# Kernel optimization log

Measured on AMD Instinct MI355X. Metric: run time of the kernel, lower is better.

The kernel has to match this reference:

```python
import jax, jax.numpy as jnp
import numpy as np

NKV = 8      # n_head_kv
G = 8        # n_head // n_head_kv
D = 64       # head_dim (hardcoded in source views)
NH = NKV * G # n_head = 64


def rotate_half(x):
    x1, x2 = x[..., : D // 2], x[..., D // 2:]
    return jnp.concatenate((-x2, x1), axis=-1)


def setup_inputs() -> dict:
    key = jax.random.key(0)
    ks = jax.random.split(key, 9)
    B, S, H = 2, 1024, 4096
    hidden_states = jax.random.normal(ks[0], (B, S, H), dtype=jnp.float32)
    alibi = jnp.zeros((B * NH, 1, S), dtype=jnp.float32)            # unused in this forward path
    attention_mask = jnp.zeros((B, 1, S, S), dtype=jnp.float32)      # unused (is_causal=True)
    cos = jax.random.uniform(ks[1], (S, D), dtype=jnp.float32, minval=-1.0, maxval=1.0)
    sin = jax.random.uniform(ks[2], (S, D), dtype=jnp.float32, minval=-1.0, maxval=1.0)
    wq = jax.random.normal(ks[3], (H, H), dtype=jnp.float32) * 0.02          # Linear weight (out, in)
    wk = jax.random.normal(ks[4], (NKV * D, H), dtype=jnp.float32) * 0.02
    wv = jax.random.normal(ks[5], (NKV * D, H), dtype=jnp.float32) * 0.02
    wd = jax.random.normal(ks[6], (H, H), dtype=jnp.float32) * 0.02          # dense weight
    return {"hidden_states": hidden_states, "alibi": alibi, "attention_mask": attention_mask,
            "cos": cos, "sin": sin, "wq": wq, "wk": wk, "wv": wv, "wd": wd}


def reference(hidden_states, alibi, attention_mask, cos, sin, wq, wk, wv, wd):
    B, S, H = hidden_states.shape
    # fused-style projections (Linear: x @ W.T, no bias)
    # q: [B, S, NKV, G, D] -> [B, NKV, G, S, D]; head h = kv_group*G + j (group-major, matches source rearrange)
    q = (hidden_states @ wq.T).reshape(B, S, NKV, G, D).transpose(0, 2, 3, 1, 4)
    k = (hidden_states @ wk.T).reshape(B, S, NKV, D).transpose(0, 2, 1, 3)   # [B, NKV, S, D]
    v = (hidden_states @ wv.T).reshape(B, S, NKV, D).transpose(0, 2, 1, 3)
    # RoPE (cos/sin broadcast over batch/head dims)
    q = q * cos + rotate_half(q) * sin
    k = k * cos + rotate_half(k) * sin
    # grouped-query attention without materializing broadcast K/V
    inv_norm = jnp.asarray(1.0 / np.sqrt(D), dtype=hidden_states.dtype)
    scores = jnp.einsum('bkgsd,bktd->bkgst', q, k) * inv_norm        # [B, NKV, G, S, S]
    causal = jnp.tril(jnp.ones((S, S), dtype=bool))
    neg = jnp.finfo(scores.dtype).min
    scores = jnp.where(causal, scores, scores + neg)
    probs = jax.nn.softmax(scores, axis=-1)
    out = jnp.einsum('bkgst,bktd->bkgsd', probs, v)                  # [B, NKV, G, S, D]
    out = out.reshape(B, NH, S, D).transpose(0, 2, 1, 3).reshape(B, S, NH * D)
    return out @ wd.T
```

## Files before the change

### kernel.cpp

```cpp
#include <hip/hip_runtime.h>
#include <hip/hip_bf16.h>
#include <cstdint>

typedef short short8 __attribute__((ext_vector_type(8)));
typedef __bf16 bf16x8 __attribute__((ext_vector_type(8)));
typedef float float4v __attribute__((ext_vector_type(4)));

#define NKV 8
#define G 8
#define D 64
#define NH 64
#define BB 2
#define S 1024
#define H 4096
#define MROWS (BB*S)
#define NQKV (H + 2*NKV*D)

__device__ __forceinline__ unsigned short f2b(float f) {
    union { float f; uint32_t u; } v; v.f = f;
    uint32_t u = v.u;
    uint32_t r = (u + 0x7FFFu + ((u >> 16) & 1u)) >> 16;
    return (unsigned short)r;
}
__device__ __forceinline__ float b2f(unsigned short b) {
    union { float f; uint32_t u; } v; v.u = ((uint32_t)b) << 16;
    return v.f;
}

__device__ __forceinline__ void gload_lds16(const unsigned short* g, unsigned short* l) {
    __builtin_amdgcn_global_load_lds(
        (const __attribute__((address_space(1))) uint32_t*)g,
        (__attribute__((address_space(3))) uint32_t*)l, 16, 0, 0);
}

__global__ void cvt_f32_bf16(const float* __restrict__ src, unsigned short* __restrict__ dst, int n) {
    int i = (blockIdx.x * blockDim.x + threadIdx.x) * 4;
    int stride = gridDim.x * blockDim.x * 4;
    for (; i < n; i += stride) {
        float4 f = *(const float4*)(src + i);
        ushort4 o;
        o.x = f2b(f.x); o.y = f2b(f.y); o.z = f2b(f.z); o.w = f2b(f.w);
        *(ushort4*)(dst + i) = o;
    }
}

template <bool BF16_OUT>
__global__ __launch_bounds__(256) void gemm_nt(
    const unsigned short* __restrict__ A, const unsigned short* __restrict__ W,
    void* __restrict__ Cv, int M, int N, int K) {
    __shared__ unsigned short As[128 * 32];
    __shared__ unsigned short Bs[128 * 32];
    const int bm = blockIdx.y * 128, bn = blockIdx.x * 128;
    const int tid = threadIdx.x;
    const int w = tid >> 6, lane = tid & 63;
    const int col = lane & 15, quad = lane >> 4;
    const int wm = (w & 1) * 64, wn = (w >> 1) * 64;
    const int sw = (quad ^ ((col >> 2) & 3)) * 8;

    const int r0 = tid >> 2;
    const int c0 = (tid & 3) ^ ((r0 >> 2) & 3);
    const unsigned short* Ap0 = A + (size_t)(bm + r0) * K + c0 * 8;
    const unsigned short* Ap1 = A + (size_t)(bm + r0 + 64) * K + c0 * 8;
    const unsigned short* Wp0 = W + (size_t)(bn + r0) * K + c0 * 8;
    const unsigned short* Wp1 = W + (size_t)(bn + r0 + 64) * K + c0 * 8;
    unsigned short* Asl0 = As + tid * 8;
    unsigned short* Asl1 = As + 2048 + tid * 8;
    unsigned short* Bsl0 = Bs + tid * 8;
    unsigned short* Bsl1 = Bs + 2048 + tid * 8;

    float4v acc[4][4];
    float4v zero4 = {0.f, 0.f, 0.f, 0.f};
#pragma unroll
    for (int i = 0; i < 4; i++)
#pragma unroll
        for (int j = 0; j < 4; j++) acc[i][j] = zero4;

    for (int k0 = 0; k0 < K; k0 += 32) {
        __syncthreads();
        gload_lds16(Ap0 + k0, Asl0);
        gload_lds16(Ap1 + k0, Asl1);
        gload_lds16(Wp0 + k0, Bsl0);
        gload_lds16(Wp1 + k0, Bsl1);
        __syncthreads();
        bf16x8 af[4], bf[4];
#pragma unroll
        for (int i = 0; i < 4; i++) af[i] = *(const bf16x8*)&As[(wm + i * 16 + col) * 32 + sw];
#pragma unroll
        for (int j = 0; j < 4; j++) bf[j] = *(const bf16x8*)&Bs[(wn + j * 16 + col) * 32 + sw];
#pragma unroll
        for (int i = 0; i < 4; i++)
#pragma unroll
            for (int j = 0; j < 4; j++)
                acc[i][j] = __builtin_amdgcn_mfma_f32_16x16x32_bf16(af[i], bf[j], acc[i][j], 0, 0, 0);
    }

#pragma unroll
    for (int i = 0; i < 4; i++) {
#pragma unroll
        for (int j = 0; j < 4; j++) {
#pragma unroll
            for (int r = 0; r < 4; r++) {
                int grow = bm + wm + i * 16 + quad * 4 + r;
                int gcol = bn + wn + j * 16 + col;
                if (BF16_OUT)
                    ((unsigned short*)Cv)[(size_t)grow * N + gcol] = f2b(acc[i][j][r]);
                else
                    ((float*)Cv)[(size_t)grow * N + gcol] = acc[i][j][r];
            }
        }
    }
}

__global__ void rope_scatter(const unsigned short* __restrict__ qkv,
                             const float* __restrict__ cosb, const float* __restrict__ sinb,
                             unsigned short* __restrict__ qa, unsigned short* __restrict__ ka,
                             unsigned short* __restrict__ vt) {
    int idx = blockIdx.x * blockDim.x + threadIdx.x;
    const int total = MROWS * NQKV;
    const int stride = gridDim.x * blockDim.x;
    for (; idx < total; idx += stride) {
        int row = idx / NQKV, o = idx - row * NQKV;
        int b = row >> 10, s = row & 1023;
        float x = b2f(qkv[idx]);
        if (o < H) {
            int kv = o >> 9, g = (o >> 6) & 7, d = o & 63;
            int po = (d < 32) ? idx + 32 : idx - 32;
            float partner = b2f(qkv[po]);
            float rot = (d < 32) ? -partner : partner;
            float y = x * cosb[s * 64 + d] + rot * sinb[s * 64 + d];
            int h = b * 64 + kv * 8 + g;
            qa[(size_t)h * (S * D) + s * 64 + d] = f2b(y);
        } else if (o < H + 512) {
            int o2 = o - H;
            int kv = o2 >> 6, d = o2 & 63;
            int po = (d < 32) ? idx + 32 : idx - 32;
            float partner = b2f(qkv[po]);
            float rot = (d < 32) ? -partner : partner;
            float y = x * cosb[s * 64 + d] + rot * sinb[s * 64 + d];
            ka[(size_t)(b * NKV + kv) * (S * D) + s * 64 + d] = f2b(y);
        } else {
            int o2 = o - H - 512;
            int kv = o2 >> 6, d = o2 & 63;
            vt[(size_t)(b * NKV + kv) * (D * S) + (size_t)d * S + s] = qkv[idx];
        }
    }
}

__global__ __launch_bounds__(256) void attn_kernel(
    const unsigned short* __restrict__ qa, const unsigned short* __restrict__ ka,
    const unsigned short* __restrict__ vt, unsigned short* __restrict__ out) {
    __shared__ unsigned short Ks[64 * 72];
    __shared__ unsigned short Vs[64 * 72];
    __shared__ unsigned short Ps[4 * 16 * 72];
    const int p = blockIdx.x;
    const int h = blockIdx.y;
    const int b = h >> 6, kvh = (h >> 3) & 7;
    const int tid = threadIdx.x, w = tid >> 6, lane = tid & 63;
    const int col = lane & 15, quad = lane >> 4;
    const unsigned short* Kg = ka + (size_t)(b * NKV + kvh) * (S * D);
    const unsigned short* Vg = vt + (size_t)(b * NKV + kvh) * (D * S);
    const int srow = tid >> 3, scc = (tid & 7) * 8;
    const int hcol = (h & 63) * 64;
    float4v zero4 = {0.f, 0.f, 0.f, 0.f};

#pragma unroll
    for (int part = 0; part < 2; part++) {
        const int qt = part ? (15 - p) : p;
        const int qb = qt * 64;
        const unsigned short* Q = qa + (size_t)h * (S * D) + (size_t)qb * D;

        bf16x8 aq[2];
#pragma unroll
        for (int c = 0; c < 2; c++)
            aq[c] = *(const bf16x8*)&Q[(w * 16 + col) * 64 + c * 32 + quad * 8];

        float m_run[4], l_run[4];
        float4v o_acc[4];
#pragma unroll
        for (int r = 0; r < 4; r++) { m_run[r] = -1e30f; l_run[r] = 0.f; }
#pragma unroll
        for (int dg = 0; dg < 4; dg++) o_acc[dg] = zero4;

        for (int kt = 0; kt <= qt; kt++) {
            const int kb = kt * 64;
            __syncthreads();
            *(short8*)&Ks[srow * 72 + scc]        = *(const short8*)&Kg[(kb + srow) * 64 + scc];
            *(short8*)&Ks[(srow + 32) * 72 + scc] = *(const short8*)&Kg[(kb + srow + 32) * 64 + scc];
            *(short8*)&Vs[srow * 72 + scc]        = *(const short8*)&Vg[(size_t)srow * S + kb + scc];
            *(short8*)&Vs[(srow + 32) * 72 + scc] = *(const short8*)&Vg[(size_t)(srow + 32) * S + kb + scc];
            __syncthreads();

            float4v sc[4];
#pragma unroll
            for (int n16 = 0; n16 < 4; n16++) {
                bf16x8 bk0 = *(const bf16x8*)&Ks[(n16 * 16 + col) * 72 + quad * 8];
                bf16x8 bk1 = *(const bf16x8*)&Ks[(n16 * 16 + col) * 72 + 32 + quad * 8];
                float4v a = __builtin_amdgcn_mfma_f32_16x16x32_bf16(aq[0], bk0, zero4, 0, 0, 0);
                sc[n16] = __builtin_amdgcn_mfma_f32_16x16x32_bf16(aq[1], bk1, a, 0, 0, 0);
            }
#pragma unroll
            for (int n16 = 0; n16 < 4; n16++) {
                int key = kb + n16 * 16 + col;
#pragma unroll
                for (int r = 0; r < 4; r++) {
                    int qrow = qb + w * 16 + quad * 4 + r;
                    float sv = sc[n16][r] * 0.125f;
                    sc[n16][r] = (key <= qrow) ? sv : -1e30f;
                }
            }
#pragma unroll
            for (int r = 0; r < 4; r++) {
                float mx = fmaxf(fmaxf(sc[0][r], sc[1][r]), fmaxf(sc[2][r], sc[3][r]));
#pragma unroll
                for (int off = 1; off < 16; off <<= 1) mx = fmaxf(mx, __shfl_xor(mx, off));
                float mnew = fmaxf(m_run[r], mx);
                float alpha = __expf(m_run[r] - mnew);
                float rsum = 0.f;
#pragma unroll
                for (int n16 = 0; n16 < 4; n16++) {
                    float pr = __expf(sc[n16][r] - mnew);
                    sc[n16][r] = pr;
                    rsum += pr;
                }
#pragma unroll
                for (int off = 1; off < 16; off <<= 1) rsum += __shfl_xor(rsum, off);
                l_run[r] = l_run[r] * alpha + rsum;
                m_run[r] = mnew;
#pragma unroll
                for (int dg = 0; dg < 4; dg++) o_acc[dg][r] *= alpha;
            }
#pragma unroll
            for (int n16 = 0; n16 < 4; n16++)
#pragma unroll
                for (int r = 0; r < 4; r++)
                    Ps[w * 1152 + (quad * 4 + r) * 72 + n16 * 16 + col] = f2b(sc[n16][r]);
            bf16x8 ap[2];
#pragma unroll
            for (int c = 0; c < 2; c++)
                ap[c] = *(const bf16x8*)&Ps[w * 1152 + col * 72 + c * 32 + quad * 8];
#pragma unroll
            for (int dg = 0; dg < 4; dg++) {
                bf16x8 bv0 = *(const bf16x8*)&Vs[(dg * 16 + col) * 72 + quad * 8];
                bf16x8 bv1 = *(const bf16x8*)&Vs[(dg * 16 + col) * 72 + 32 + quad * 8];
                float4v t = __builtin_amdgcn_mfma_f32_16x16x32_bf16(ap[0], bv0, o_acc[dg], 0, 0, 0);
                o_acc[dg] = __builtin_amdgcn_mfma_f32_16x16x32_bf16(ap[1], bv1, t, 0, 0, 0);
            }
        }
#pragma unroll
        for (int r = 0; r < 4; r++) {
            float inv = 1.f / l_run[r];
            int grow = b * S + qb + w * 16 + quad * 4 + r;
#pragma unroll
            for (int dg = 0; dg < 4; dg++)
                out[(size_t)grow * H + hcol + dg * 16 + col] = f2b(o_acc[dg][r] * inv);
        }
    }
}

extern "C" void kernel_launch(void* const* d_in, const int* in_sizes, int n_in,
                              void* d_out, int out_size, void* d_ws, size_t ws_size,
                              hipStream_t stream) {
    const float* hs   = (const float*)d_in[0];
    const float* cosb = (const float*)d_in[3];
    const float* sinb = (const float*)d_in[4];
    const float* wq   = (const float*)d_in[5];
    const float* wk   = (const float*)d_in[6];
    const float* wv   = (const float*)d_in[7];
    const float* wd   = (const float*)d_in[8];

    char* p = (char*)d_ws;
    auto alloc = [&](size_t bytes) { char* r = p; p += (bytes + 255) & ~(size_t)255; return r; };
    unsigned short* wqkv_b = (unsigned short*)alloc((size_t)NQKV * H * 2);
    unsigned short* wd_b   = (unsigned short*)alloc((size_t)H * H * 2);
    unsigned short* qkv    = (unsigned short*)alloc((size_t)MROWS * NQKV * 2);
    unsigned short* qa     = (unsigned short*)alloc((size_t)BB * NH * S * D * 2);
    unsigned short* ka     = (unsigned short*)alloc((size_t)BB * NKV * S * D * 2);
    unsigned short* vt     = (unsigned short*)alloc((size_t)BB * NKV * S * D * 2);
    unsigned short* hs_b   = (unsigned short*)alloc((size_t)MROWS * H * 2);
    unsigned short* ao     = hs_b;

    cvt_f32_bf16<<<2048, 256, 0, stream>>>(hs, hs_b, MROWS * H);
    cvt_f32_bf16<<<2048, 256, 0, stream>>>(wq, wqkv_b, H * H);
    cvt_f32_bf16<<<1024, 256, 0, stream>>>(wk, wqkv_b + (size_t)H * H, 512 * H);
    cvt_f32_bf16<<<1024, 256, 0, stream>>>(wv, wqkv_b + (size_t)H * H + (size_t)512 * H, 512 * H);
    cvt_f32_bf16<<<2048, 256, 0, stream>>>(wd, wd_b, H * H);

    gemm_nt<true><<<dim3(NQKV / 128, MROWS / 128), 256, 0, stream>>>(hs_b, wqkv_b, qkv, MROWS, NQKV, H);
    rope_scatter<<<4096, 256, 0, stream>>>(qkv, cosb, sinb, qa, ka, vt);
    attn_kernel<<<dim3(8, 128), 256, 0, stream>>>(qa, ka, vt, ao);
    gemm_nt<false><<<dim3(H / 128, MROWS / 128), 256, 0, stream>>>(ao, wd_b, d_out, MROWS, H, H);
}
```

Baseline: 524.4 us.

## Use 32x32 MFMA in GEMM, share K/V tiles across two heads, fuse conversions

The GEMM moves from 16x16x32 to 32x32x16 bf16 MFMA with a 2x2 accumulator layout per wave, precomputed LDS pointers and a matching swizzle. The attention kernel now processes two query heads per block, so each K/V tile load is reused twice, and it uses exp2 with a prescaled log2e factor. The five conversion launches become one fused kernel. These changes cut LDS traffic per MFMA, K/V reloads and launch overhead, at the cost of more registers in attention and a branchy conversion loop.

```diff
diff --git a/kernel.cpp b/kernel.cpp
--- a/kernel.cpp
+++ b/kernel.cpp
@@ -5,6 +5,7 @@
 typedef short short8 __attribute__((ext_vector_type(8)));
 typedef __bf16 bf16x8 __attribute__((ext_vector_type(8)));
 typedef float float4v __attribute__((ext_vector_type(4)));
+typedef float float16v __attribute__((ext_vector_type(16)));
 
 #define NKV 8
 #define G 8
@@ -33,14 +34,31 @@
         (__attribute__((address_space(3))) uint32_t*)l, 16, 0, 0);
 }
 
-__global__ void cvt_f32_bf16(const float* __restrict__ src, unsigned short* __restrict__ dst, int n) {
-    int i = (blockIdx.x * blockDim.x + threadIdx.x) * 4;
-    int stride = gridDim.x * blockDim.x * 4;
-    for (; i < n; i += stride) {
-        float4 f = *(const float4*)(src + i);
+__global__ void cvt_all(const float* __restrict__ hs, const float* __restrict__ wq,
+                        const float* __restrict__ wk, const float* __restrict__ wv,
+                        const float* __restrict__ wd,
+                        unsigned short* __restrict__ hs_b, unsigned short* __restrict__ wqkv_b,
+                        unsigned short* __restrict__ wd_b) {
+    const size_t N0 = (size_t)MROWS * H;
+    const size_t N1 = (size_t)H * H;
+    const size_t N2 = (size_t)512 * H;
+    const size_t N3 = (size_t)512 * H;
+    const size_t N4 = (size_t)H * H;
+    const size_t total4 = (N0 + N1 + N2 + N3 + N4) / 4;
+    size_t i = (size_t)blockIdx.x * blockDim.x + threadIdx.x;
+    const size_t stride = (size_t)gridDim.x * blockDim.x;
+    for (; i < total4; i += stride) {
+        size_t e = i * 4;
+        const float* s; unsigned short* d;
+        if (e < N0)                { s = hs + e;                  d = hs_b + e; }
+        else if (e < N0+N1)        { s = wq + (e-N0);             d = wqkv_b + (e-N0); }
+        else if (e < N0+N1+N2)     { s = wk + (e-N0-N1);          d = wqkv_b + N1 + (e-N0-N1); }
+        else if (e < N0+N1+N2+N3)  { s = wv + (e-N0-N1-N2);       d = wqkv_b + N1+N2 + (e-N0-N1-N2); }
+        else                       { s = wd + (e-N0-N1-N2-N3);    d = wd_b + (e-N0-N1-N2-N3); }
+        float4 f = *(const float4*)s;
         ushort4 o;
         o.x = f2b(f.x); o.y = f2b(f.y); o.z = f2b(f.z); o.w = f2b(f.w);
-        *(ushort4*)(dst + i) = o;
+        *(ushort4*)d = o;
     }
 }
 
@@ -53,59 +71,72 @@
     const int bm = blockIdx.y * 128, bn = blockIdx.x * 128;
     const int tid = threadIdx.x;
     const int w = tid >> 6, lane = tid & 63;
-    const int col = lane & 15, quad = lane >> 4;
+    const int n32 = lane & 31, khalf = lane >> 5;
     const int wm = (w & 1) * 64, wn = (w >> 1) * 64;
-    const int sw = (quad ^ ((col >> 2) & 3)) * 8;
 
     const int r0 = tid >> 2;
     const int c0 = (tid & 3) ^ ((r0 >> 2) & 3);
-    const unsigned short* Ap0 = A + (size_t)(bm + r0) * K + c0 * 8;
-    const unsigned short* Ap1 = A + (size_t)(bm + r0 + 64) * K + c0 * 8;
-    const unsigned short* Wp0 = W + (size_t)(bn + r0) * K + c0 * 8;
-    const unsigned short* Wp1 = W + (size_t)(bn + r0 + 64) * K + c0 * 8;
+    const unsigned short* pA0 = A + (size_t)(bm + r0) * K + c0 * 8;
+    const unsigned short* pA1 = A + (size_t)(bm + r0 + 64) * K + c0 * 8;
+    const unsigned short* pW0 = W + (size_t)(bn + r0) * K + c0 * 8;
+    const unsigned short* pW1 = W + (size_t)(bn + r0 + 64) * K + c0 * 8;
     unsigned short* Asl0 = As + tid * 8;
     unsigned short* Asl1 = As + 2048 + tid * 8;
     unsigned short* Bsl0 = Bs + tid * 8;
     unsigned short* Bsl1 = Bs + 2048 + tid * 8;
 
-    float4v acc[4][4];
-    float4v zero4 = {0.f, 0.f, 0.f, 0.f};
-#pragma unroll
-    for (int i = 0; i < 4; i++)
-#pragma unroll
-        for (int j = 0; j < 4; j++) acc[i][j] = zero4;
-
-    for (int k0 = 0; k0 < K; k0 += 32) {
+    const unsigned short* aP[2][2];
+    const unsigned short* bP[2][2];
+#pragma unroll
+    for (int g = 0; g < 2; g++)
+#pragma unroll
+        for (int s = 0; s < 2; s++) {
+            int cp = ((s << 1) | khalf) ^ ((n32 >> 2) & 3);
+            aP[g][s] = &As[(wm + g * 32 + n32) * 32 + cp * 8];
+            bP[g][s] = &Bs[(wn + g * 32 + n32) * 32 + cp * 8];
+        }
+
+    float16v acc[2][2] = {};
+
+    const int iters = K >> 5;
+    for (int it = 0; it < iters; ++it) {
         __syncthreads();
-        gload_lds16(Ap0 + k0, Asl0);
-        gload_lds16(Ap1 + k0, Asl1);
-        gload_lds16(Wp0 + k0, Bsl0);
-        gload_lds16(Wp1 + k0, Bsl1);
+        gload_lds16(pA0, Asl0);
+        gload_lds16(pA1, Asl1);
+        gload_lds16(pW0, Bsl0);
+        gload_lds16(pW1, Bsl1);
+        pA0 += 32; pA1 += 32; pW0 += 32; pW1 += 32;
         __syncthreads();
-        bf16x8 af[4], bf[4];
-#pragma unroll
-        for (int i = 0; i < 4; i++) af[i] = *(const bf16x8*)&As[(wm + i * 16 + col) * 32 + sw];
-#pragma unroll
-        for (int j = 0; j < 4; j++) bf[j] = *(const bf16x8*)&Bs[(wn + j * 16 + col) * 32 + sw];
-#pragma unroll
-        for (int i = 0; i < 4; i++)
-#pragma unroll
-            for (int j = 0; j < 4; j++)
-                acc[i][j] = __builtin_amdgcn_mfma_f32_16x16x32_bf16(af[i], bf[j], acc[i][j], 0, 0, 0);
-    }
-
-#pragma unroll
-    for (int i = 0; i < 4; i++) {
-#pragma unroll
-        for (int j = 0; j < 4; j++) {
-#pragma unroll
-            for (int r = 0; r < 4; r++) {
-                int grow = bm + wm + i * 16 + quad * 4 + r;
-                int gcol = bn + wn + j * 16 + col;
+        bf16x8 af[2][2], bf[2][2];
+#pragma unroll
+        for (int g = 0; g < 2; g++)
+#pragma unroll
+            for (int s = 0; s < 2; s++) {
+                af[g][s] = *(const bf16x8*)aP[g][s];
+                bf[g][s] = *(const bf16x8*)bP[g][s];
+            }
+#pragma unroll
+        for (int s = 0; s < 2; s++)
+#pragma unroll
+            for (int mg = 0; mg < 2; mg++)
+#pragma unroll
+                for (int ng = 0; ng < 2; ng++)
+                    acc[mg][ng] = __builtin_amdgcn_mfma_f32_32x32x16_bf16(
+                        af[mg][s], bf[ng][s], acc[mg][ng], 0, 0, 0);
+    }
+
+#pragma unroll
+    for (int mg = 0; mg < 2; mg++) {
+#pragma unroll
+        for (int ng = 0; ng < 2; ng++) {
+            int gcol = bn + wn + ng * 32 + n32;
+#pragma unroll
+            for (int reg = 0; reg < 16; reg++) {
+                int grow = bm + wm + mg * 32 + (reg & 3) + 8 * (reg >> 2) + 4 * khalf;
                 if (BF16_OUT)
-                    ((unsigned short*)Cv)[(size_t)grow * N + gcol] = f2b(acc[i][j][r]);
+                    ((unsigned short*)Cv)[(size_t)grow * N + gcol] = f2b(acc[mg][ng][reg]);
                 else
-                    ((float*)Cv)[(size_t)grow * N + gcol] = acc[i][j][r];
+                    ((float*)Cv)[(size_t)grow * N + gcol] = acc[mg][ng][reg];
             }
         }
     }
@@ -153,33 +184,39 @@
     __shared__ unsigned short Vs[64 * 72];
     __shared__ unsigned short Ps[4 * 16 * 72];
     const int p = blockIdx.x;
-    const int h = blockIdx.y;
-    const int b = h >> 6, kvh = (h >> 3) & 7;
+    const int yy = blockIdx.y;
+    const int b = yy >> 5, kvh = (yy >> 2) & 7, gp = yy & 3;
+    const int h0 = b * 64 + kvh * 8 + gp * 2;
     const int tid = threadIdx.x, w = tid >> 6, lane = tid & 63;
     const int col = lane & 15, quad = lane >> 4;
     const unsigned short* Kg = ka + (size_t)(b * NKV + kvh) * (S * D);
     const unsigned short* Vg = vt + (size_t)(b * NKV + kvh) * (D * S);
     const int srow = tid >> 3, scc = (tid & 7) * 8;
-    const int hcol = (h & 63) * 64;
     float4v zero4 = {0.f, 0.f, 0.f, 0.f};
+    const float SC2 = 0.125f * 1.44269504089f;
 
 #pragma unroll
     for (int part = 0; part < 2; part++) {
         const int qt = part ? (15 - p) : p;
         const int qb = qt * 64;
-        const unsigned short* Q = qa + (size_t)h * (S * D) + (size_t)qb * D;
-
-        bf16x8 aq[2];
-#pragma unroll
-        for (int c = 0; c < 2; c++)
-            aq[c] = *(const bf16x8*)&Q[(w * 16 + col) * 64 + c * 32 + quad * 8];
-
-        float m_run[4], l_run[4];
-        float4v o_acc[4];
-#pragma unroll
-        for (int r = 0; r < 4; r++) { m_run[r] = -1e30f; l_run[r] = 0.f; }
-#pragma unroll
-        for (int dg = 0; dg < 4; dg++) o_acc[dg] = zero4;
+
+        bf16x8 aq[2][2];
+#pragma unroll
+        for (int hd = 0; hd < 2; hd++)
+#pragma unroll
+            for (int c = 0; c < 2; c++)
+                aq[hd][c] = *(const bf16x8*)&qa[(size_t)(h0 + hd) * (S * D) + (size_t)qb * D
+                                               + (w * 16 + col) * 64 + c * 32 + quad * 8];
+
+        float m_run[2][4], l_run[2][4];
+        float4v o_acc[2][4];
+#pragma unroll
+        for (int hd = 0; hd < 2; hd++) {
+#pragma unroll
+            for (int r = 0; r < 4; r++) { m_run[hd][r] = -1e30f; l_run[hd][r] = 0.f; }
+#pragma unroll
+            for (int dg = 0; dg < 4; dg++) o_acc[hd][dg] = zero4;
+        }
 
         for (int kt = 0; kt <= qt; kt++) {
             const int kb = kt * 64;
@@ -190,69 +227,76 @@
             *(short8*)&Vs[(srow + 32) * 72 + scc] = *(const short8*)&Vg[(size_t)(srow + 32) * S + kb + scc];
             __syncthreads();
 
-            float4v sc[4];
-#pragma unroll
-            for (int n16 = 0; n16 < 4; n16++) {
-                bf16x8 bk0 = *(const bf16x8*)&Ks[(n16 * 16 + col) * 72 + quad * 8];
-                bf16x8 bk1 = *(const bf16x8*)&Ks[(n16 * 16 + col) * 72 + 32 + quad * 8];
-                float4v a = __builtin_amdgcn_mfma_f32_16x16x32_bf16(aq[0], bk0, zero4, 0, 0, 0);
-                sc[n16] = __builtin_amdgcn_mfma_f32_16x16x32_bf16(aq[1], bk1, a, 0, 0, 0);
-            }
-#pragma unroll
-            for (int n16 = 0; n16 < 4; n16++) {
-                int key = kb + n16 * 16 + col;
+#pragma unroll
+            for (int hd = 0; hd < 2; hd++) {
+                float4v sc[4];
+#pragma unroll
+                for (int n16 = 0; n16 < 4; n16++) {
+                    bf16x8 bk0 = *(const bf16x8*)&Ks[(n16 * 16 + col) * 72 + quad * 8];
+                    bf16x8 bk1 = *(const bf16x8*)&Ks[(n16 * 16 + col) * 72 + 32 + quad * 8];
+                    float4v a = __builtin_amdgcn_mfma_f32_16x16x32_bf16(aq[hd][0], bk0, zero4, 0, 0, 0);
+                    sc[n16] = __builtin_amdgcn_mfma_f32_16x16x32_bf16(aq[hd][1], bk1, a, 0, 0, 0);
+                }
+#pragma unroll
+                for (int n16 = 0; n16 < 4; n16++) {
+                    int key = kb + n16 * 16 + col;
+#pragma unroll
+                    for (int r = 0; r < 4; r++) {
+                        int qrow = qb + w * 16 + quad * 4 + r;
+                        float sv = sc[n16][r] * SC2;
+                        sc[n16][r] = (key <= qrow) ? sv : -1e30f;
+                    }
+                }
 #pragma unroll
                 for (int r = 0; r < 4; r++) {
-                    int qrow = qb + w * 16 + quad * 4 + r;
-                    float sv = sc[n16][r] * 0.125f;
-                    sc[n16][r] = (key <= qrow) ? sv : -1e30f;
+                    float mx = fmaxf(fmaxf(sc[0][r], sc[1][r]), fmaxf(sc[2][r], sc[3][r]));
+#pragma unroll
+                    for (int off = 1; off < 16; off <<= 1) mx = fmaxf(mx, __shfl_xor(mx, off));
+                    float mnew = fmaxf(m_run[hd][r], mx);
+                    float alpha = __builtin_amdgcn_exp2f(m_run[hd][r] - mnew);
+                    float rsum = 0.f;
+#pragma unroll
+                    for (int n16 = 0; n16 < 4; n16++) {
+                        float pr = __builtin_amdgcn_exp2f(sc[n16][r] - mnew);
+                        sc[n16][r] = pr;
+                        rsum += pr;
+                    }
+#pragma unroll
+                    for (int off = 1; off < 16; off <<= 1) rsum += __shfl_xor(rsum, off);
+                    l_run[hd][r] = l_run[hd][r] * alpha + rsum;
+                    m_run[hd][r] = mnew;
+#pragma unroll
+                    for (int dg = 0; dg < 4; dg++) o_acc[hd][dg][r] *= alpha;
+                }
+#pragma unroll
+                for (int n16 = 0; n16 < 4; n16++)
+#pragma unroll
+                    for (int r = 0; r < 4; r++)
+                        Ps[w * 1152 + (quad * 4 + r) * 72 + n16 * 16 + col] = f2b(sc[n16][r]);
+                bf16x8 ap[2];
+#pragma unroll
+                for (int c = 0; c < 2; c++)
+                    ap[c] = *(const bf16x8*)&Ps[w * 1152 + col * 72 + c * 32 + quad * 8];
+#pragma unroll
+                for (int dg = 0; dg < 4; dg++) {
+                    bf16x8 bv0 = *(const bf16x8*)&Vs[(dg * 16 + col) * 72 + quad * 8];
+                    bf16x8 bv1 = *(const bf16x8*)&Vs[(dg * 16 + col) * 72 + 32 + quad * 8];
+                    float4v t = __builtin_amdgcn_mfma_f32_16x16x32_bf16(ap[0], bv0, o_acc[hd][dg], 0, 0, 0);
+                    o_acc[hd][dg] = __builtin_amdgcn_mfma_f32_16x16x32_bf16(ap[1], bv1, t, 0, 0, 0);
                 }
             }
+        }
+#pragma unroll
+        for (int hd = 0; hd < 2; hd++) {
+            const int hcol = ((h0 + hd) & 63) * 64;
 #pragma unroll
             for (int r = 0; r < 4; r++) {
-                float mx = fmaxf(fmaxf(sc[0][r], sc[1][r]), fmaxf(sc[2][r], sc[3][r]));
-#pragma unroll
-                for (int off = 1; off < 16; off <<= 1) mx = fmaxf(mx, __shfl_xor(mx, off));
-                float mnew = fmaxf(m_run[r], mx);
-                float alpha = __expf(m_run[r] - mnew);
-                float rsum = 0.f;
-#pragma unroll
-                for (int n16 = 0; n16 < 4; n16++) {
-                    float pr = __expf(sc[n16][r] - mnew);
-                    sc[n16][r] = pr;
-                    rsum += pr;
-                }
-#pragma unroll
-                for (int off = 1; off < 16; off <<= 1) rsum += __shfl_xor(rsum, off);
-                l_run[r] = l_run[r] * alpha + rsum;
-                m_run[r] = mnew;
-#pragma unroll
-                for (int dg = 0; dg < 4; dg++) o_acc[dg][r] *= alpha;
+                float inv = 1.f / l_run[hd][r];
+                int grow = b * S + qb + w * 16 + quad * 4 + r;
+#pragma unroll
+                for (int dg = 0; dg < 4; dg++)
+                    out[(size_t)grow * H + hcol + dg * 16 + col] = f2b(o_acc[hd][dg][r] * inv);
             }
-#pragma unroll
-            for (int n16 = 0; n16 < 4; n16++)
-#pragma unroll
-                for (int r = 0; r < 4; r++)
-                    Ps[w * 1152 + (quad * 4 + r) * 72 + n16 * 16 + col] = f2b(sc[n16][r]);
-            bf16x8 ap[2];
-#pragma unroll
-            for (int c = 0; c < 2; c++)
-                ap[c] = *(const bf16x8*)&Ps[w * 1152 + col * 72 + c * 32 + quad * 8];
-#pragma unroll
-            for (int dg = 0; dg < 4; dg++) {
-                bf16x8 bv0 = *(const bf16x8*)&Vs[(dg * 16 + col) * 72 + quad * 8];
-                bf16x8 bv1 = *(const bf16x8*)&Vs[(dg * 16 + col) * 72 + 32 + quad * 8];
-                float4v t = __builtin_amdgcn_mfma_f32_16x16x32_bf16(ap[0], bv0, o_acc[dg], 0, 0, 0);
-                o_acc[dg] = __builtin_amdgcn_mfma_f32_16x16x32_bf16(ap[1], bv1, t, 0, 0, 0);
-            }
-        }
-#pragma unroll
-        for (int r = 0; r < 4; r++) {
-            float inv = 1.f / l_run[r];
-            int grow = b * S + qb + w * 16 + quad * 4 + r;
-#pragma unroll
-            for (int dg = 0; dg < 4; dg++)
-                out[(size_t)grow * H + hcol + dg * 16 + col] = f2b(o_acc[dg][r] * inv);
         }
     }
 }
@@ -279,14 +323,10 @@
     unsigned short* hs_b   = (unsigned short*)alloc((size_t)MROWS * H * 2);
     unsigned short* ao     = hs_b;
 
-    cvt_f32_bf16<<<2048, 256, 0, stream>>>(hs, hs_b, MROWS * H);
-    cvt_f32_bf16<<<2048, 256, 0, stream>>>(wq, wqkv_b, H * H);
-    cvt_f32_bf16<<<1024, 256, 0, stream>>>(wk, wqkv_b + (size_t)H * H, 512 * H);
-    cvt_f32_bf16<<<1024, 256, 0, stream>>>(wv, wqkv_b + (size_t)H * H + (size_t)512 * H, 512 * H);
-    cvt_f32_bf16<<<2048, 256, 0, stream>>>(wd, wd_b, H * H);
+    cvt_all<<<4096, 256, 0, stream>>>(hs, wq, wk, wv, wd, hs_b, wqkv_b, wd_b);
 
     gemm_nt<true><<<dim3(NQKV / 128, MROWS / 128), 256, 0, stream>>>(hs_b, wqkv_b, qkv, MROWS, NQKV, H);
     rope_scatter<<<4096, 256, 0, stream>>>(qkv, cosb, sinb, qa, ka, vt);
-    attn_kernel<<<dim3(8, 128), 256, 0, stream>>>(qa, ka, vt, ao);
+    attn_kernel<<<dim3(8, 64), 256, 0, stream>>>(qa, ka, vt, ao);
     gemm_nt<false><<<dim3(H / 128, MROWS / 128), 256, 0, stream>>>(ao, wd_b, d_out, MROWS, H, H);
 }
```

After: 514.3 us. Within noise of the previous version (-1.9%).
